# Performance work log

Measured on AMD Instinct MI355X. Metric: run time of the kernel, lower is better.

## Reference

```python
import jax, jax.numpy as jnp
import numpy as np

N = 50000      # nodes per graph
E = 800000     # edges per graph (avg degree 16)
IN = 128       # in_channels == hidden_channels
HID = 128      # out_channels (heads=1)
R = 8          # num_relations
NEG = 0.2      # PyG RGATConv default negative_slope


def setup_inputs() -> dict:
    key = jax.random.key(0)
    ks = jax.random.split(key, 14)
    s_w = (2.0 / (IN + HID)) ** 0.5  # glorot-ish scale
    return {
        "x_one": jax.random.normal(ks[0], (N, IN), jnp.float32),
        "edge_index_one": jax.random.randint(ks[1], (2, E), 0, N),
        "edge_type_one": jax.random.randint(ks[2], (E,), 0, R),
        "x_two": jax.random.normal(ks[3], (N, IN), jnp.float32),
        "edge_index_two": jax.random.randint(ks[4], (2, E), 0, N),
        "edge_type_two": jax.random.randint(ks[5], (E,), 0, R),
        "W1": jax.random.normal(ks[6], (R, IN, HID), jnp.float32) * s_w,
        "q1": jax.random.normal(ks[7], (HID, 1), jnp.float32) * s_w,
        "k1": jax.random.normal(ks[8], (HID, 1), jnp.float32) * s_w,
        "b1": jnp.zeros((HID,), jnp.float32),
        "W2": jax.random.normal(ks[9], (R, IN, HID), jnp.float32) * s_w,
        "q2": jax.random.normal(ks[10], (HID, 1), jnp.float32) * s_w,
        "k2": jax.random.normal(ks[11], (HID, 1), jnp.float32) * s_w,
        "b2": jnp.zeros((HID,), jnp.float32),
    }


def _rgat(x, edge_index, edge_type, W, q, k, b):
    """PyG RGATConv (heads=1, additive-self-attention, across-relation)."""
    n = x.shape[0]
    src, dst = edge_index[0], edge_index[1]
    # per-relation linear transform of all nodes: [R, N, HID]
    xt = jnp.einsum('nd,rdo->rno', x, W)
    out_i = xt[edge_type, dst]   # [E, HID] transformed target (x_i W_r)
    out_j = xt[edge_type, src]   # [E, HID] transformed source (x_j W_r)
    qi = out_i @ q               # [E, 1]
    kj = out_j @ k               # [E, 1]
    alpha = jax.nn.leaky_relu(qi + kj, NEG)
    # scatter-softmax over incoming edges of each dst node
    amax = jax.ops.segment_max(alpha, dst, num_segments=n)
    amax = jnp.where(jnp.isfinite(amax), amax, 0.0)
    ex = jnp.exp(alpha - amax[dst])
    denom = jax.ops.segment_sum(ex, dst, num_segments=n) + 1e-16
    a = ex / denom[dst]          # [E, 1]
    # weighted scatter-add aggregation + bias
    out = jax.ops.segment_sum(a * out_j, dst, num_segments=n) + b
    return out


def reference(x_one, edge_index_one, edge_type_one,
              x_two, edge_index_two, edge_type_two,
              W1, q1, k1, b1, W2, q2, k2, b2):
    o1 = jax.nn.relu(_rgat(x_one, edge_index_one, edge_type_one, W1, q1, k1, b1))
    o2 = jax.nn.relu(_rgat(x_two, edge_index_two, edge_type_two, W2, q2, k2, b2))
    return (o1, o2)
```

## Files before the change

kernel.cpp:

```cpp
#include <hip/hip_runtime.h>


typedef unsigned short u16;
typedef __attribute__((ext_vector_type(8))) short short8;
typedef __attribute__((ext_vector_type(4))) float floatx4;
typedef __attribute__((ext_vector_type(4))) float float4v;
typedef __attribute__((ext_vector_type(4))) unsigned uint4v;

__device__ __forceinline__ u16 f2bf(float f) {
  union { float f; unsigned u; } v; v.f = f;
  unsigned r = v.u + 0x7FFFu + ((v.u >> 16) & 1u);
  return (u16)(r >> 16);
}
__device__ __forceinline__ float bflo(unsigned v) {
  union { unsigned u; float f; } c; c.u = v << 16; return c.f;
}
__device__ __forceinline__ float bfhi(unsigned v) {
  union { unsigned u; float f; } c; c.u = v & 0xffff0000u; return c.f;
}

__global__ void k_prep_wb(const float* __restrict__ W1, const float* __restrict__ W2,
                          u16* __restrict__ Wb, int KK) {
  int t = blockIdx.x * 256 + threadIdx.x;
  int lane = t & 63, nt = (t >> 6) & 7, kk = t >> 9;
  if (kk >= KK) return;
  const float* W = blockIdx.y ? W2 : W1;
  u16* out = Wb + (size_t)blockIdx.y * KK * 4096;
  int q = lane >> 4, m16 = lane & 15;
  int c = nt * 16 + m16;
  short8 v;
#pragma unroll
  for (int j = 0; j < 8; ++j) {
    int k = kk * 32 + q * 8 + j;
    v[j] = (short)f2bf(W[(size_t)k * 128 + c]);
  }
  *(short8*)(out + (size_t)t * 8) = v;
}

__global__ void k_prep_wqk(const float* __restrict__ W1, const float* __restrict__ q1,
                           const float* __restrict__ k1, const float* __restrict__ W2,
                           const float* __restrict__ q2, const float* __restrict__ k2,
                           float* __restrict__ Wq, float* __restrict__ Wk, int RD) {
  int wid = (blockIdx.x * 256 + threadIdx.x) >> 6;
  int lane = threadIdx.x & 63;
  if (wid >= 2 * RD) return;
  int g = wid >= RD;
  const float* W = g ? W2 : W1;
  const float* qv = g ? q2 : q1;
  const float* kv = g ? k2 : k1;
  const float* row = W + (size_t)(wid - g * RD) * 128;
  float a0 = row[lane], a1 = row[lane + 64];
  float vq = a0 * qv[lane] + a1 * qv[lane + 64];
  float vk = a0 * kv[lane] + a1 * kv[lane + 64];
#pragma unroll
  for (int off = 32; off; off >>= 1) {
    vq += __shfl_xor(vq, off);
    vk += __shfl_xor(vk, off);
  }
  if (lane == 0) { Wq[wid] = vq; Wk[wid] = vk; }
}

__global__ void k_prep_bqk(const float* __restrict__ Wq, const float* __restrict__ Wk,
                           u16* __restrict__ Bqk, int R) {
  int total = 2 * 4 * 64 * 8;
  for (int idx = threadIdx.x; idx < total; idx += 256) {
    int j = idx & 7, lane = (idx >> 3) & 63, kk = (idx >> 9) & 3, g = idx >> 11;
    int k = kk * 32 + ((lane >> 4) & 3) * 8 + j;
    int n = lane & 15;
    float v = (n < 8) ? Wq[(g * R + n) * 128 + k] : Wk[(g * R + (n & 7)) * 128 + k];
    Bqk[idx] = f2bf(v);
  }
}

__global__ void __launch_bounds__(256) k_count(
    const int* __restrict__ d1, const int* __restrict__ d2,
    int* __restrict__ gcnt, int N, int E, int NB) {
  __shared__ int h[512];
  int tid = threadIdx.x;
  for (int i = tid; i < NB; i += 256) h[i] = 0;
  __syncthreads();
  int E2 = 2 * E;
  int e0 = blockIdx.x * 4096;
#pragma unroll
  for (int j = 0; j < 16; ++j) {
    int e = e0 + j * 256 + tid;
    if (e < E2) {
      int g = e >= E;
      int d = g ? d2[e - E] : d1[e];
      atomicAdd(&h[(g * N + d) >> 8], 1);
    }
  }
  __syncthreads();
  for (int i = tid; i < NB; i += 256)
    if (h[i]) atomicAdd(&gcnt[i], h[i]);
}

__global__ void k_bucket_scan(const int* __restrict__ gcnt, int* __restrict__ bbase,
                              int* __restrict__ bcur, int* __restrict__ offs,
                              int NB, int total, int N2) {
  __shared__ int sd[512];
  int tid = threadIdx.x;
  int v0 = (tid < NB) ? gcnt[tid] : 0;
  int v1 = (tid + 256 < NB) ? gcnt[tid + 256] : 0;
  sd[tid] = v0; sd[tid + 256] = v1;
  __syncthreads();
  for (int off = 1; off < 512; off <<= 1) {
    int t0 = (tid >= off) ? sd[tid - off] : 0;
    int t1 = (tid + 256 >= off) ? sd[tid + 256 - off] : 0;
    __syncthreads();
    sd[tid] += t0; sd[tid + 256] += t1;
    __syncthreads();
  }
  if (tid < NB) { int b = sd[tid] - v0; bbase[tid] = b; bcur[tid] = b; }
  if (tid + 256 < NB) { int b = sd[tid + 256] - v1; bbase[tid + 256] = b; bcur[tid + 256] = b; }
  if (tid == 0) { bbase[NB] = total; offs[N2] = total; }
}

__global__ void __launch_bounds__(256) k_bin(
    const int* __restrict__ ei1, const int* __restrict__ et1,
    const int* __restrict__ ei2, const int* __restrict__ et2,
    int* __restrict__ bcur, uint2* __restrict__ staged, int N, int E, int NB) {
  __shared__ int hist[512];
  __shared__ int basev[512];
  __shared__ int runstart[512];
  __shared__ unsigned sta[4096 * 2];
  int tid = threadIdx.x;
  int E2 = 2 * E;
  int e0 = blockIdx.x * 4096;
  int cnt2 = min(4096, E2 - e0);
  for (int i = tid; i < 512; i += 256) hist[i] = 0;
  __syncthreads();
  int dstg[16], srcet[16], rank[16];
#pragma unroll
  for (int j = 0; j < 16; ++j) {
    int e = e0 + j * 256 + tid;
    dstg[j] = -1;
    if (e < E2) {
      int g = e >= E;
      int el = e - (g ? E : 0);
      const int* ei = g ? ei2 : ei1;
      int s = ei[el], d = ei[E + el];
      int etv = (g ? et2 : et1)[el];
      dstg[j] = g * N + d;
      srcet[j] = (s << 3) | etv;
      rank[j] = atomicAdd(&hist[dstg[j] >> 8], 1);
    }
  }
  __syncthreads();
  basev[tid] = hist[tid];
  basev[tid + 256] = hist[tid + 256];
  __syncthreads();
  for (int off = 1; off < 512; off <<= 1) {
    int i0 = tid, i1 = tid + 256;
    int v0 = (i0 >= off) ? basev[i0 - off] : 0;
    int v1 = (i1 >= off) ? basev[i1 - off] : 0;
    __syncthreads();
    basev[i0] += v0; basev[i1] += v1;
    __syncthreads();
  }
  for (int i = tid; i < NB; i += 256)
    if (hist[i] > 0) runstart[i] = atomicAdd(&bcur[i], hist[i]);
  __syncthreads();
#pragma unroll
  for (int j = 0; j < 16; ++j)
    if (dstg[j] >= 0) {
      int b = dstg[j] >> 8;
      int slot = basev[b] - hist[b] + rank[j];
      sta[slot * 2] = (unsigned)dstg[j];
      sta[slot * 2 + 1] = (unsigned)srcet[j];
    }
  __syncthreads();
  for (int i = tid; i < cnt2; i += 256) {
    unsigned dg = sta[i * 2], se = sta[i * 2 + 1];
    int b = (int)(dg >> 8);
    int dest = runstart[b] + (i - (basev[b] - hist[b]));
    staged[dest] = make_uint2(dg, se);
  }
}

__global__ void __launch_bounds__(256) k_scatter2(
    const uint2* __restrict__ staged, const int* __restrict__ bbase,
    int* __restrict__ offs, int* __restrict__ csr, int N2) {
  __shared__ int hist[256];
  __shared__ int sd[256];
  __shared__ int cur[256];
  int b = blockIdx.x, tid = threadIdx.x;
  int nb0 = b << 8;
  int nnode = min(256, N2 - nb0);
  int s0 = bbase[b], s1 = bbase[b + 1];
  hist[tid] = 0;
  __syncthreads();
  for (int i = s0 + tid; i < s1; i += 256)
    atomicAdd(&hist[(int)staged[i].x - nb0], 1);
  __syncthreads();
  int v = hist[tid];
  sd[tid] = v; __syncthreads();
  for (int off = 1; off < 256; off <<= 1) {
    int t = (tid >= off) ? sd[tid - off] : 0;
    __syncthreads();
    sd[tid] += t;
    __syncthreads();
  }
  int ex = sd[tid] - v;
  if (tid < nnode) offs[nb0 + tid] = s0 + ex;
  cur[tid] = ex;
  __syncthreads();
  for (int i = s0 + tid; i < s1; i += 256) {
    uint2 en = staged[i];
    int node = (int)en.x - nb0;
    int sl = atomicAdd(&cur[node], 1);
    csr[s0 + sl] = (int)en.y;
  }
}

__global__ void __launch_bounds__(256) k_gemm_xt(
    const float* __restrict__ x, const u16* __restrict__ Wb,
    const u16* __restrict__ Bqk, u16* __restrict__ xt,
    float* __restrict__ sq, float* __restrict__ sk,
    int N, int R, int node_base) {
  __shared__ u16 st[4][2][2048];
  int wave = threadIdx.x >> 6, lane = threadIdx.x & 63;
  int m0 = blockIdx.x * 64 + wave * 16;
  int rbase = blockIdx.y * 4;
  int q = lane >> 4, m16 = lane & 15;
  int node = m0 + m16;
  int srow = (node < N) ? node : N - 1;
  short8 bfrag[4];
#pragma unroll
  for (int kk = 0; kk < 4; ++kk) {
    const float* ap = x + (size_t)srow * 128 + kk * 32 + q * 8;
    float4v f0 = *(const float4v*)ap;
    float4v f1 = *(const float4v*)(ap + 4);
    short8 a;
    a[0] = (short)f2bf(f0.x); a[1] = (short)f2bf(f0.y);
    a[2] = (short)f2bf(f0.z); a[3] = (short)f2bf(f0.w);
    a[4] = (short)f2bf(f1.x); a[5] = (short)f2bf(f1.y);
    a[6] = (short)f2bf(f1.z); a[7] = (short)f2bf(f1.w);
    bfrag[kk] = a;
  }
  if (blockIdx.y == 0) {
    floatx4 accq = (floatx4){0.f, 0.f, 0.f, 0.f};
#pragma unroll
    for (int kk = 0; kk < 4; ++kk) {
      short8 aq = *(const short8*)(Bqk + (size_t)kk * 512 + lane * 8);
      accq = __builtin_amdgcn_mfma_f32_16x16x32_bf16(aq, bfrag[kk], accq, 0, 0, 0);
    }
    if (node < N) {
      float* dst = (q < 2 ? sq : sk) + (size_t)(node_base + node) * 8 + (q & 1) * 4;
      *(float4v*)dst = (float4v){accq[0], accq[1], accq[2], accq[3]};
    }
  }
#pragma unroll
  for (int rr = 0; rr < 4; ++rr) {
    int r = rbase + rr;
    u16* s = st[wave][rr & 1];
    floatx4 acc[8];
#pragma unroll
    for (int nt = 0; nt < 8; ++nt) acc[nt] = (floatx4){0.f, 0.f, 0.f, 0.f};
#pragma unroll
    for (int kk = 0; kk < 4; ++kk) {
      const u16* wbp = Wb + ((size_t)((r * 4 + kk) * 8) * 64 + lane) * 8;
#pragma unroll
      for (int nt = 0; nt < 8; ++nt) {
        short8 a = *(const short8*)(wbp + nt * 512);
        acc[nt] = __builtin_amdgcn_mfma_f32_16x16x32_bf16(a, bfrag[kk], acc[nt], 0, 0, 0);
      }
    }
#pragma unroll
    for (int nt = 0; nt < 8; ++nt) {
      union { u16 h[4]; unsigned long long u; } pk;
      pk.h[0] = f2bf(acc[nt][0]); pk.h[1] = f2bf(acc[nt][1]);
      pk.h[2] = f2bf(acc[nt][2]); pk.h[3] = f2bf(acc[nt][3]);
      int c16 = 2 * nt + (q >> 1);
      *(unsigned long long*)(s + (((m16 << 4) + (c16 ^ m16)) << 3) + ((q & 1) << 2)) = pk.u;
    }
#pragma unroll
    for (int it = 0; it < 4; ++it) {
      int rl = it * 4 + q;
      int gm = m0 + rl;
      if (gm < N) {
        uint4v vv = *(const uint4v*)(s + (((rl << 4) + (m16 ^ rl)) << 3));
        *(uint4v*)(xt + ((size_t)r * N + gm) * 128 + m16 * 8) = vv;
      }
    }
  }
}

__global__ void __launch_bounds__(256) k_aggregate(
    const int* __restrict__ csr, const int* __restrict__ offs,
    const float* __restrict__ sq, const float* __restrict__ sk,
    const u16* __restrict__ xt, const float* __restrict__ bias,
    float* __restrict__ out, int N, int node_base) {
  int nl = blockIdx.x * 4 + (threadIdx.x >> 6);
  int lane = threadIdx.x & 63;
  if (nl >= N) return;
  int node = node_base + nl;
  int start = offs[node], end = offs[node + 1];
  const float* sqn = sq + (size_t)node * 8;

  float al[8]; int pl[8];
  float m = -INFINITY;
  {
    int c = 0;
    for (int i = start + lane; i < end; i += 64, ++c) {
      int p = csr[i]; int s = p >> 3, e = p & 7;
      float a = sqn[e] + sk[(size_t)(node_base + s) * 8 + e];
      a = (a > 0.f) ? a : 0.2f * a;
      if (c < 8) { al[c] = a; pl[c] = p; }
      m = fmaxf(m, a);
    }
  }
#pragma unroll
  for (int off = 32; off; off >>= 1) m = fmaxf(m, __shfl_xor(m, off));

  float ssum = 0.f;
  {
    int c = 0;
    for (int i = start + lane; i < end; i += 64, ++c) {
      float a;
      if (c < 8) a = al[c];
      else {
        int p = csr[i]; int s = p >> 3, e = p & 7;
        a = sqn[e] + sk[(size_t)(node_base + s) * 8 + e];
        a = (a > 0.f) ? a : 0.2f * a;
      }
      ssum += __expf(a - m);
    }
  }
#pragma unroll
  for (int off = 32; off; off >>= 1) ssum += __shfl_xor(ssum, off);
  float inv = 1.f / (ssum + 1e-16f);

  float acc0 = 0.f, acc1 = 0.f;
  const char* xtb = (const char*)xt;
  int c = 0;
  for (int base = start; base < end; base += 64, ++c) {
    int cnt = min(64, end - base);
    float w = 0.f; int b = 0;
    {
      int i = base + lane;
      if (i < end) {
        int p; float a;
        if (c < 8) { p = pl[c]; a = al[c]; }
        else {
          p = csr[i]; int s = p >> 3, e = p & 7;
          a = sqn[e] + sk[(size_t)(node_base + s) * 8 + e];
          a = (a > 0.f) ? a : 0.2f * a;
        }
        w = __expf(a - m) * inv;
        b = ((p & 7) * N + (p >> 3)) << 8;
      }
    }
    int j = 0;
    for (; j + 3 < cnt; j += 4) {
      float w0 = __shfl(w, j), w1 = __shfl(w, j + 1),
            w2 = __shfl(w, j + 2), w3 = __shfl(w, j + 3);
      int b0 = __shfl(b, j), b1 = __shfl(b, j + 1),
          b2 = __shfl(b, j + 2), b3 = __shfl(b, j + 3);
      unsigned v0 = *(const unsigned*)(xtb + b0 + lane * 4);
      unsigned v1 = *(const unsigned*)(xtb + b1 + lane * 4);
      unsigned v2 = *(const unsigned*)(xtb + b2 + lane * 4);
      unsigned v3 = *(const unsigned*)(xtb + b3 + lane * 4);
      acc0 += w0 * bflo(v0); acc1 += w0 * bfhi(v0);
      acc0 += w1 * bflo(v1); acc1 += w1 * bfhi(v1);
      acc0 += w2 * bflo(v2); acc1 += w2 * bfhi(v2);
      acc0 += w3 * bflo(v3); acc1 += w3 * bfhi(v3);
    }
    for (; j < cnt; ++j) {
      float w0 = __shfl(w, j);
      int b0 = __shfl(b, j);
      unsigned v0 = *(const unsigned*)(xtb + b0 + lane * 4);
      acc0 += w0 * bflo(v0); acc1 += w0 * bfhi(v0);
    }
  }
  float o0 = fmaxf(acc0 + bias[lane * 2], 0.f);
  float o1 = fmaxf(acc1 + bias[lane * 2 + 1], 0.f);
  union { float f[2]; unsigned long long u; } pk;
  pk.f[0] = o0; pk.f[1] = o1;
  __builtin_nontemporal_store(pk.u,
      (unsigned long long*)(out + (size_t)nl * 128 + lane * 2));
}

extern "C" void kernel_launch(void* const* d_in, const int* in_sizes, int n_in,
                              void* d_out, int out_size, void* d_ws, size_t ws_size,
                              hipStream_t stream) {
  const float* x1 = (const float*)d_in[0];
  const int* ei1 = (const int*)d_in[1];
  const int* et1 = (const int*)d_in[2];
  const float* x2 = (const float*)d_in[3];
  const int* ei2 = (const int*)d_in[4];
  const int* et2 = (const int*)d_in[5];
  const float* W1 = (const float*)d_in[6];
  const float* q1 = (const float*)d_in[7];
  const float* k1 = (const float*)d_in[8];
  const float* b1 = (const float*)d_in[9];
  const float* W2 = (const float*)d_in[10];
  const float* q2 = (const float*)d_in[11];
  const float* k2 = (const float*)d_in[12];
  const float* b2 = (const float*)d_in[13];

  const int N = in_sizes[0] / 128;
  const int E = in_sizes[1] / 2;
  const int R = in_sizes[6] / (128 * 128);
  const int KK = R * 4;
  const int N2 = 2 * N;
  const int NB = (N2 + 255) >> 8;

  size_t off = 0;
  char* w = (char*)d_ws;
  auto carve = [&](size_t bytes) -> void* {
    void* p = w + off;
    off += (bytes + 255) & ~(size_t)255;
    return p;
  };
  u16* xt = (u16*)carve((size_t)R * N * 128 * 2);
  uint2* staged = (uint2*)xt;
  u16* Wb = (u16*)carve((size_t)2 * KK * 4096 * 2);
  u16* Bqk = (u16*)carve((size_t)2 * 4 * 64 * 8 * 2);
  float* Wq = (float*)carve((size_t)2 * R * 128 * 4);
  float* Wk = (float*)carve((size_t)2 * R * 128 * 4);
  float* sq = (float*)carve((size_t)N2 * 8 * 4);
  float* sk = (float*)carve((size_t)N2 * 8 * 4);
  int* offs = (int*)carve((size_t)(N2 + 1) * 4);
  int* gcnt = (int*)carve(512 * 4);
  int* bbase = (int*)carve(520 * 4);
  int* bcur = (int*)carve(512 * 4);
  int* csr = (int*)carve((size_t)2 * E * 4);
  if (off > ws_size) return;

  const int nbin = (2 * E + 4095) / 4096;

  hipMemsetAsync(gcnt, 0, 512 * 4, stream);
  k_prep_wb<<<dim3((KK * 512 + 255) / 256, 2), dim3(256), 0, stream>>>(W1, W2, Wb, KK);
  k_prep_wqk<<<dim3((2 * R * 128 * 64 + 255) / 256), dim3(256), 0, stream>>>(
      W1, q1, k1, W2, q2, k2, Wq, Wk, R * 128);
  k_prep_bqk<<<dim3(1), dim3(256), 0, stream>>>(Wq, Wk, Bqk, R);
  k_count<<<dim3(nbin), dim3(256), 0, stream>>>(ei1 + E, ei2 + E, gcnt, N, E, NB);
  k_bucket_scan<<<dim3(1), dim3(256), 0, stream>>>(gcnt, bbase, bcur, offs, NB, 2 * E, N2);
  k_bin<<<dim3(nbin), dim3(256), 0, stream>>>(ei1, et1, ei2, et2, bcur, staged, N, E, NB);
  k_scatter2<<<dim3(NB), dim3(256), 0, stream>>>(staged, bbase, offs, csr, N2);

  for (int g = 0; g < 2; ++g) {
    const float* x = g ? x2 : x1;
    const float* bv = g ? b2 : b1;
    float* outp = (float*)d_out + (size_t)g * N * 128;
    k_gemm_xt<<<dim3((N + 63) / 64, 2), dim3(256), 0, stream>>>(
        x, Wb + (size_t)g * KK * 4096, Bqk + (size_t)g * 2048, xt,
        sq, sk, N, R, g * N);
    k_aggregate<<<dim3((N + 3) / 4), dim3(256), 0, stream>>>(
        csr, offs, sq, sk, xt, bv, outp, N, g * N);
  }
}
```

Measured before the change: 356.1 us.

## Replace bucketed two-pass CSR build with per-node count, scan and atomic placement

The CSR build used a two-level scheme: coarse bucket histograms, LDS-staged binning into 256-node buckets, then a per-bucket scatter pass. It becomes per-node global atomic counts, a three-kernel exclusive scan over 100k nodes, and a single placement pass using global atomics on per-node cursors. This removes the staged intermediate buffer and its extra read/write pass. In exchange it adds more global atomics and kernel launches, and edge order within each node becomes nondeterministic, which may change float summation order and aggregation locality.

```diff
diff --git a/kernel.cpp b/kernel.cpp
--- a/kernel.cpp
+++ b/kernel.cpp
@@ -74,34 +74,45 @@
 
 __global__ void __launch_bounds__(256) k_count(
     const int* __restrict__ d1, const int* __restrict__ d2,
-    int* __restrict__ gcnt, int N, int E, int NB) {
-  __shared__ int h[512];
-  int tid = threadIdx.x;
-  for (int i = tid; i < NB; i += 256) h[i] = 0;
-  __syncthreads();
+    int* __restrict__ nodecnt, int N, int E) {
   int E2 = 2 * E;
   int e0 = blockIdx.x * 4096;
 #pragma unroll
   for (int j = 0; j < 16; ++j) {
-    int e = e0 + j * 256 + tid;
+    int e = e0 + j * 256 + threadIdx.x;
     if (e < E2) {
       int g = e >= E;
       int d = g ? d2[e - E] : d1[e];
-      atomicAdd(&h[(g * N + d) >> 8], 1);
-    }
-  }
+      atomicAdd(&nodecnt[g * N + d], 1);
+    }
+  }
+}
+
+__global__ void __launch_bounds__(256) k_scan1(
+    const int* __restrict__ nodecnt, int* __restrict__ exls,
+    int* __restrict__ bsum, int N2) {
+  __shared__ int sd[256];
+  int tid = threadIdx.x;
+  int n = (blockIdx.x << 8) + tid;
+  int v = (n < N2) ? nodecnt[n] : 0;
+  sd[tid] = v;
   __syncthreads();
-  for (int i = tid; i < NB; i += 256)
-    if (h[i]) atomicAdd(&gcnt[i], h[i]);
-}
-
-__global__ void k_bucket_scan(const int* __restrict__ gcnt, int* __restrict__ bbase,
-                              int* __restrict__ bcur, int* __restrict__ offs,
-                              int NB, int total, int N2) {
+  for (int off = 1; off < 256; off <<= 1) {
+    int t = (tid >= off) ? sd[tid - off] : 0;
+    __syncthreads();
+    sd[tid] += t;
+    __syncthreads();
+  }
+  if (n < N2) exls[n] = sd[tid] - v;
+  if (tid == 255) bsum[blockIdx.x] = sd[255];
+}
+
+__global__ void k_scan2(const int* __restrict__ bsum, int* __restrict__ bbase,
+                        int* __restrict__ offs, int NB, int total, int N2) {
   __shared__ int sd[512];
   int tid = threadIdx.x;
-  int v0 = (tid < NB) ? gcnt[tid] : 0;
-  int v1 = (tid + 256 < NB) ? gcnt[tid + 256] : 0;
+  int v0 = (tid < NB) ? bsum[tid] : 0;
+  int v1 = (tid + 256 < NB) ? bsum[tid + 256] : 0;
   sd[tid] = v0; sd[tid + 256] = v1;
   __syncthreads();
   for (int off = 1; off < 512; off <<= 1) {
@@ -111,105 +122,40 @@
     sd[tid] += t0; sd[tid + 256] += t1;
     __syncthreads();
   }
-  if (tid < NB) { int b = sd[tid] - v0; bbase[tid] = b; bcur[tid] = b; }
-  if (tid + 256 < NB) { int b = sd[tid + 256] - v1; bbase[tid + 256] = b; bcur[tid + 256] = b; }
+  if (tid < NB) bbase[tid] = sd[tid] - v0;
+  if (tid + 256 < NB) bbase[tid + 256] = sd[tid + 256] - v1;
   if (tid == 0) { bbase[NB] = total; offs[N2] = total; }
 }
 
-__global__ void __launch_bounds__(256) k_bin(
+__global__ void __launch_bounds__(256) k_scan3(
+    const int* __restrict__ exls, const int* __restrict__ bbase,
+    int* __restrict__ offs, int* __restrict__ cur, int N2) {
+  int n = (blockIdx.x << 8) + threadIdx.x;
+  if (n < N2) {
+    int v = bbase[blockIdx.x] + exls[n];
+    offs[n] = v;
+    cur[n] = v;
+  }
+}
+
+__global__ void __launch_bounds__(256) k_place(
     const int* __restrict__ ei1, const int* __restrict__ et1,
     const int* __restrict__ ei2, const int* __restrict__ et2,
-    int* __restrict__ bcur, uint2* __restrict__ staged, int N, int E, int NB) {
-  __shared__ int hist[512];
-  __shared__ int basev[512];
-  __shared__ int runstart[512];
-  __shared__ unsigned sta[4096 * 2];
-  int tid = threadIdx.x;
+    int* __restrict__ cur, int* __restrict__ csr, int N, int E) {
   int E2 = 2 * E;
   int e0 = blockIdx.x * 4096;
-  int cnt2 = min(4096, E2 - e0);
-  for (int i = tid; i < 512; i += 256) hist[i] = 0;
-  __syncthreads();
-  int dstg[16], srcet[16], rank[16];
 #pragma unroll
   for (int j = 0; j < 16; ++j) {
-    int e = e0 + j * 256 + tid;
-    dstg[j] = -1;
+    int e = e0 + j * 256 + threadIdx.x;
     if (e < E2) {
       int g = e >= E;
       int el = e - (g ? E : 0);
       const int* ei = g ? ei2 : ei1;
       int s = ei[el], d = ei[E + el];
       int etv = (g ? et2 : et1)[el];
-      dstg[j] = g * N + d;
-      srcet[j] = (s << 3) | etv;
-      rank[j] = atomicAdd(&hist[dstg[j] >> 8], 1);
-    }
-  }
-  __syncthreads();
-  basev[tid] = hist[tid];
-  basev[tid + 256] = hist[tid + 256];
-  __syncthreads();
-  for (int off = 1; off < 512; off <<= 1) {
-    int i0 = tid, i1 = tid + 256;
-    int v0 = (i0 >= off) ? basev[i0 - off] : 0;
-    int v1 = (i1 >= off) ? basev[i1 - off] : 0;
-    __syncthreads();
-    basev[i0] += v0; basev[i1] += v1;
-    __syncthreads();
-  }
-  for (int i = tid; i < NB; i += 256)
-    if (hist[i] > 0) runstart[i] = atomicAdd(&bcur[i], hist[i]);
-  __syncthreads();
-#pragma unroll
-  for (int j = 0; j < 16; ++j)
-    if (dstg[j] >= 0) {
-      int b = dstg[j] >> 8;
-      int slot = basev[b] - hist[b] + rank[j];
-      sta[slot * 2] = (unsigned)dstg[j];
-      sta[slot * 2 + 1] = (unsigned)srcet[j];
-    }
-  __syncthreads();
-  for (int i = tid; i < cnt2; i += 256) {
-    unsigned dg = sta[i * 2], se = sta[i * 2 + 1];
-    int b = (int)(dg >> 8);
-    int dest = runstart[b] + (i - (basev[b] - hist[b]));
-    staged[dest] = make_uint2(dg, se);
-  }
-}
-
-__global__ void __launch_bounds__(256) k_scatter2(
-    const uint2* __restrict__ staged, const int* __restrict__ bbase,
-    int* __restrict__ offs, int* __restrict__ csr, int N2) {
-  __shared__ int hist[256];
-  __shared__ int sd[256];
-  __shared__ int cur[256];
-  int b = blockIdx.x, tid = threadIdx.x;
-  int nb0 = b << 8;
-  int nnode = min(256, N2 - nb0);
-  int s0 = bbase[b], s1 = bbase[b + 1];
-  hist[tid] = 0;
-  __syncthreads();
-  for (int i = s0 + tid; i < s1; i += 256)
-    atomicAdd(&hist[(int)staged[i].x - nb0], 1);
-  __syncthreads();
-  int v = hist[tid];
-  sd[tid] = v; __syncthreads();
-  for (int off = 1; off < 256; off <<= 1) {
-    int t = (tid >= off) ? sd[tid - off] : 0;
-    __syncthreads();
-    sd[tid] += t;
-    __syncthreads();
-  }
-  int ex = sd[tid] - v;
-  if (tid < nnode) offs[nb0 + tid] = s0 + ex;
-  cur[tid] = ex;
-  __syncthreads();
-  for (int i = s0 + tid; i < s1; i += 256) {
-    uint2 en = staged[i];
-    int node = (int)en.x - nb0;
-    int sl = atomicAdd(&cur[node], 1);
-    csr[s0 + sl] = (int)en.y;
+      int slot = atomicAdd(&cur[g * N + d], 1);
+      csr[slot] = (s << 3) | etv;
+    }
   }
 }
 
@@ -414,7 +360,6 @@
     return p;
   };
   u16* xt = (u16*)carve((size_t)R * N * 128 * 2);
-  uint2* staged = (uint2*)xt;
   u16* Wb = (u16*)carve((size_t)2 * KK * 4096 * 2);
   u16* Bqk = (u16*)carve((size_t)2 * 4 * 64 * 8 * 2);
   float* Wq = (float*)carve((size_t)2 * R * 128 * 4);
@@ -422,23 +367,26 @@
   float* sq = (float*)carve((size_t)N2 * 8 * 4);
   float* sk = (float*)carve((size_t)N2 * 8 * 4);
   int* offs = (int*)carve((size_t)(N2 + 1) * 4);
-  int* gcnt = (int*)carve(512 * 4);
+  int* nodecnt = (int*)carve((size_t)N2 * 4);
+  int* exls = (int*)carve((size_t)N2 * 4);
+  int* cur = (int*)carve((size_t)N2 * 4);
+  int* bsum = (int*)carve(512 * 4);
   int* bbase = (int*)carve(520 * 4);
-  int* bcur = (int*)carve(512 * 4);
   int* csr = (int*)carve((size_t)2 * E * 4);
   if (off > ws_size) return;
 
   const int nbin = (2 * E + 4095) / 4096;
 
-  hipMemsetAsync(gcnt, 0, 512 * 4, stream);
+  hipMemsetAsync(nodecnt, 0, (size_t)N2 * 4, stream);
   k_prep_wb<<<dim3((KK * 512 + 255) / 256, 2), dim3(256), 0, stream>>>(W1, W2, Wb, KK);
   k_prep_wqk<<<dim3((2 * R * 128 * 64 + 255) / 256), dim3(256), 0, stream>>>(
       W1, q1, k1, W2, q2, k2, Wq, Wk, R * 128);
   k_prep_bqk<<<dim3(1), dim3(256), 0, stream>>>(Wq, Wk, Bqk, R);
-  k_count<<<dim3(nbin), dim3(256), 0, stream>>>(ei1 + E, ei2 + E, gcnt, N, E, NB);
-  k_bucket_scan<<<dim3(1), dim3(256), 0, stream>>>(gcnt, bbase, bcur, offs, NB, 2 * E, N2);
-  k_bin<<<dim3(nbin), dim3(256), 0, stream>>>(ei1, et1, ei2, et2, bcur, staged, N, E, NB);
-  k_scatter2<<<dim3(NB), dim3(256), 0, stream>>>(staged, bbase, offs, csr, N2);
+  k_count<<<dim3(nbin), dim3(256), 0, stream>>>(ei1 + E, ei2 + E, nodecnt, N, E);
+  k_scan1<<<dim3(NB), dim3(256), 0, stream>>>(nodecnt, exls, bsum, N2);
+  k_scan2<<<dim3(1), dim3(256), 0, stream>>>(bsum, bbase, offs, NB, 2 * E, N2);
+  k_scan3<<<dim3(NB), dim3(256), 0, stream>>>(exls, bbase, offs, cur, N2);
+  k_place<<<dim3(nbin), dim3(256), 0, stream>>>(ei1, et1, ei2, et2, cur, csr, N, E);
 
   for (int g = 0; g < 2; ++g) {
     const float* x = g ? x2 : x1;
```

After: 489.6 us. +37.5%, slower.

## Batch both graphs into single GEMM and aggregate launches, fuse Wq/Wk prep

Applied to the files above, without the earlier changes.

When the workspace can hold two copies of the transformed node features, the two graphs are processed by one k_gemm_xt launch and one k_aggregate launch, with the graph index taken from a grid dimension. Otherwise the old per-graph loop is kept. The Wq/Wk projection and Bqk packing kernels are merged into a single multi-block kernel, and f32-to-bf16 conversion now uses the packed v_cvt_pk_bf16_f32 instruction. This cuts launch count and serialization between graphs and gives each launch more parallelism, at the cost of twice the workspace for xt and less L2 reuse per graph.

```diff
diff --git a/kernel.cpp b/kernel.cpp
--- a/kernel.cpp
+++ b/kernel.cpp
@@ -17,6 +17,11 @@
 }
 __device__ __forceinline__ float bfhi(unsigned v) {
   union { unsigned u; float f; } c; c.u = v & 0xffff0000u; return c.f;
+}
+__device__ __forceinline__ unsigned cvtpk(float lo, float hi) {
+  unsigned r;
+  asm("v_cvt_pk_bf16_f32 %0, %1, %2" : "=v"(r) : "v"(lo), "v"(hi));
+  return r;
 }
 
 __global__ void k_prep_wb(const float* __restrict__ W1, const float* __restrict__ W2,
@@ -37,39 +42,26 @@
   *(short8*)(out + (size_t)t * 8) = v;
 }
 
-__global__ void k_prep_wqk(const float* __restrict__ W1, const float* __restrict__ q1,
-                           const float* __restrict__ k1, const float* __restrict__ W2,
-                           const float* __restrict__ q2, const float* __restrict__ k2,
-                           float* __restrict__ Wq, float* __restrict__ Wk, int RD) {
-  int wid = (blockIdx.x * 256 + threadIdx.x) >> 6;
-  int lane = threadIdx.x & 63;
-  if (wid >= 2 * RD) return;
-  int g = wid >= RD;
+__global__ void __launch_bounds__(256) k_prep_bqk(
+    const float* __restrict__ W1, const float* __restrict__ q1,
+    const float* __restrict__ k1, const float* __restrict__ W2,
+    const float* __restrict__ q2, const float* __restrict__ k2,
+    u16* __restrict__ Bqk) {
+  int idx = blockIdx.x * 256 + threadIdx.x;
+  int j = idx & 7, lane = (idx >> 3) & 63, kk = (idx >> 9) & 3, g = idx >> 11;
+  int k = kk * 32 + ((lane >> 4) & 3) * 8 + j;
+  int n = lane & 15;
   const float* W = g ? W2 : W1;
-  const float* qv = g ? q2 : q1;
-  const float* kv = g ? k2 : k1;
-  const float* row = W + (size_t)(wid - g * RD) * 128;
-  float a0 = row[lane], a1 = row[lane + 64];
-  float vq = a0 * qv[lane] + a1 * qv[lane + 64];
-  float vk = a0 * kv[lane] + a1 * kv[lane + 64];
-#pragma unroll
-  for (int off = 32; off; off >>= 1) {
-    vq += __shfl_xor(vq, off);
-    vk += __shfl_xor(vk, off);
-  }
-  if (lane == 0) { Wq[wid] = vq; Wk[wid] = vk; }
-}
-
-__global__ void k_prep_bqk(const float* __restrict__ Wq, const float* __restrict__ Wk,
-                           u16* __restrict__ Bqk, int R) {
-  int total = 2 * 4 * 64 * 8;
-  for (int idx = threadIdx.x; idx < total; idx += 256) {
-    int j = idx & 7, lane = (idx >> 3) & 63, kk = (idx >> 9) & 3, g = idx >> 11;
-    int k = kk * 32 + ((lane >> 4) & 3) * 8 + j;
-    int n = lane & 15;
-    float v = (n < 8) ? Wq[(g * R + n) * 128 + k] : Wk[(g * R + (n & 7)) * 128 + k];
-    Bqk[idx] = f2bf(v);
-  }
+  const float* vec = (n < 8) ? (g ? q2 : q1) : (g ? k2 : k1);
+  const float* row = W + ((size_t)(n & 7) * 128 + k) * 128;
+  float s = 0.f;
+#pragma unroll
+  for (int o = 0; o < 128; o += 4) {
+    float4v wv = *(const float4v*)(row + o);
+    float4v qv = *(const float4v*)(vec + o);
+    s += wv.x * qv.x + wv.y * qv.y + wv.z * qv.z + wv.w * qv.w;
+  }
+  Bqk[idx] = f2bf(s);
 }
 
 __global__ void __launch_bounds__(256) k_count(
@@ -214,11 +206,18 @@
 }
 
 __global__ void __launch_bounds__(256) k_gemm_xt(
-    const float* __restrict__ x, const u16* __restrict__ Wb,
-    const u16* __restrict__ Bqk, u16* __restrict__ xt,
+    const float* __restrict__ x1, const float* __restrict__ x2,
+    const u16* __restrict__ Wb, const u16* __restrict__ Bqk,
+    u16* __restrict__ xt, unsigned long long xt_gstride,
     float* __restrict__ sq, float* __restrict__ sk,
-    int N, int R, int node_base) {
+    int N, int R, int g0) {
   __shared__ u16 st[4][2][2048];
+  int g = g0 + blockIdx.z;
+  const float* x = g ? x2 : x1;
+  const u16* Wbg = Wb + (size_t)g * (R * 4) * 4096;
+  const u16* Bqkg = Bqk + (size_t)g * 2048;
+  u16* xtg = xt + (size_t)g * xt_gstride;
+  int node_base = g * N;
   int wave = threadIdx.x >> 6, lane = threadIdx.x & 63;
   int m0 = blockIdx.x * 64 + wave * 16;
   int rbase = blockIdx.y * 4;
@@ -231,18 +230,16 @@
     const float* ap = x + (size_t)srow * 128 + kk * 32 + q * 8;
     float4v f0 = *(const float4v*)ap;
     float4v f1 = *(const float4v*)(ap + 4);
-    short8 a;
-    a[0] = (short)f2bf(f0.x); a[1] = (short)f2bf(f0.y);
-    a[2] = (short)f2bf(f0.z); a[3] = (short)f2bf(f0.w);
-    a[4] = (short)f2bf(f1.x); a[5] = (short)f2bf(f1.y);
-    a[6] = (short)f2bf(f1.z); a[7] = (short)f2bf(f1.w);
-    bfrag[kk] = a;
+    union { unsigned u[4]; short8 s; } pb;
+    pb.u[0] = cvtpk(f0.x, f0.y); pb.u[1] = cvtpk(f0.z, f0.w);
+    pb.u[2] = cvtpk(f1.x, f1.y); pb.u[3] = cvtpk(f1.z, f1.w);
+    bfrag[kk] = pb.s;
   }
   if (blockIdx.y == 0) {
     floatx4 accq = (floatx4){0.f, 0.f, 0.f, 0.f};
 #pragma unroll
     for (int kk = 0; kk < 4; ++kk) {
-      short8 aq = *(const short8*)(Bqk + (size_t)kk * 512 + lane * 8);
+      short8 aq = *(const short8*)(Bqkg + (size_t)kk * 512 + lane * 8);
       accq = __builtin_amdgcn_mfma_f32_16x16x32_bf16(aq, bfrag[kk], accq, 0, 0, 0);
     }
     if (node < N) {
@@ -259,7 +256,7 @@
     for (int nt = 0; nt < 8; ++nt) acc[nt] = (floatx4){0.f, 0.f, 0.f, 0.f};
 #pragma unroll
     for (int kk = 0; kk < 4; ++kk) {
-      const u16* wbp = Wb + ((size_t)((r * 4 + kk) * 8) * 64 + lane) * 8;
+      const u16* wbp = Wbg + ((size_t)((r * 4 + kk) * 8) * 64 + lane) * 8;
 #pragma unroll
       for (int nt = 0; nt < 8; ++nt) {
         short8 a = *(const short8*)(wbp + nt * 512);
@@ -268,11 +265,11 @@
     }
 #pragma unroll
     for (int nt = 0; nt < 8; ++nt) {
-      union { u16 h[4]; unsigned long long u; } pk;
-      pk.h[0] = f2bf(acc[nt][0]); pk.h[1] = f2bf(acc[nt][1]);
-      pk.h[2] = f2bf(acc[nt][2]); pk.h[3] = f2bf(acc[nt][3]);
+      union { unsigned u[2]; unsigned long long ull; } pk;
+      pk.u[0] = cvtpk(acc[nt][0], acc[nt][1]);
+      pk.u[1] = cvtpk(acc[nt][2], acc[nt][3]);
       int c16 = 2 * nt + (q >> 1);
-      *(unsigned long long*)(s + (((m16 << 4) + (c16 ^ m16)) << 3) + ((q & 1) << 2)) = pk.u;
+      *(unsigned long long*)(s + (((m16 << 4) + (c16 ^ m16)) << 3) + ((q & 1) << 2)) = pk.ull;
     }
 #pragma unroll
     for (int it = 0; it < 4; ++it) {
@@ -280,7 +277,7 @@
       int gm = m0 + rl;
       if (gm < N) {
         uint4v vv = *(const uint4v*)(s + (((rl << 4) + (m16 ^ rl)) << 3));
-        *(uint4v*)(xt + ((size_t)r * N + gm) * 128 + m16 * 8) = vv;
+        *(uint4v*)(xtg + ((size_t)r * N + gm) * 128 + m16 * 8) = vv;
       }
     }
   }
@@ -289,11 +286,17 @@
 __global__ void __launch_bounds__(256) k_aggregate(
     const int* __restrict__ csr, const int* __restrict__ offs,
     const float* __restrict__ sq, const float* __restrict__ sk,
-    const u16* __restrict__ xt, const float* __restrict__ bias,
-    float* __restrict__ out, int N, int node_base) {
+    const u16* __restrict__ xt, unsigned long long xt_gstride,
+    const float* __restrict__ b1, const float* __restrict__ b2,
+    float* __restrict__ out, int N, int g0) {
   int nl = blockIdx.x * 4 + (threadIdx.x >> 6);
   int lane = threadIdx.x & 63;
   if (nl >= N) return;
+  int g = g0 + blockIdx.y;
+  int node_base = g * N;
+  const float* bias = g ? b2 : b1;
+  const u16* xtg = xt + (size_t)g * xt_gstride;
+  float* outp = out + (size_t)g * N * 128;
   int node = node_base + nl;
   int start = offs[node], end = offs[node + 1];
   const float* sqn = sq + (size_t)node * 8;
@@ -332,7 +335,7 @@
   float inv = 1.f / (ssum + 1e-16f);
 
   float acc0 = 0.f, acc1 = 0.f;
-  const char* xtb = (const char*)xt;
+  const char* xtb = (const char*)xtg;
   int c = 0;
   for (int base = start; base < end; base += 64, ++c) {
     int cnt = min(64, end - base);
@@ -355,11 +358,11 @@
     for (; j + 3 < cnt; j += 4) {
       float w0 = __shfl(w, j), w1 = __shfl(w, j + 1),
             w2 = __shfl(w, j + 2), w3 = __shfl(w, j + 3);
-      int b0 = __shfl(b, j), b1 = __shfl(b, j + 1),
-          b2 = __shfl(b, j + 2), b3 = __shfl(b, j + 3);
+      int b0 = __shfl(b, j), b1_ = __shfl(b, j + 1),
+          b2_ = __shfl(b, j + 2), b3 = __shfl(b, j + 3);
       unsigned v0 = *(const unsigned*)(xtb + b0 + lane * 4);
-      unsigned v1 = *(const unsigned*)(xtb + b1 + lane * 4);
-      unsigned v2 = *(const unsigned*)(xtb + b2 + lane * 4);
+      unsigned v1 = *(const unsigned*)(xtb + b1_ + lane * 4);
+      unsigned v2 = *(const unsigned*)(xtb + b2_ + lane * 4);
       unsigned v3 = *(const unsigned*)(xtb + b3 + lane * 4);
       acc0 += w0 * bflo(v0); acc1 += w0 * bfhi(v0);
       acc0 += w1 * bflo(v1); acc1 += w1 * bfhi(v1);
@@ -378,7 +381,7 @@
   union { float f[2]; unsigned long long u; } pk;
   pk.f[0] = o0; pk.f[1] = o1;
   __builtin_nontemporal_store(pk.u,
-      (unsigned long long*)(out + (size_t)nl * 128 + lane * 2));
+      (unsigned long long*)(outp + (size_t)nl * 128 + lane * 2));
 }
 
 extern "C" void kernel_launch(void* const* d_in, const int* in_sizes, int n_in,
@@ -413,12 +416,8 @@
     off += (bytes + 255) & ~(size_t)255;
     return p;
   };
-  u16* xt = (u16*)carve((size_t)R * N * 128 * 2);
-  uint2* staged = (uint2*)xt;
   u16* Wb = (u16*)carve((size_t)2 * KK * 4096 * 2);
   u16* Bqk = (u16*)carve((size_t)2 * 4 * 64 * 8 * 2);
-  float* Wq = (float*)carve((size_t)2 * R * 128 * 4);
-  float* Wk = (float*)carve((size_t)2 * R * 128 * 4);
   float* sq = (float*)carve((size_t)N2 * 8 * 4);
   float* sk = (float*)carve((size_t)N2 * 8 * 4);
   int* offs = (int*)carve((size_t)(N2 + 1) * 4);
@@ -426,28 +425,34 @@
   int* bbase = (int*)carve(520 * 4);
   int* bcur = (int*)carve(512 * 4);
   int* csr = (int*)carve((size_t)2 * E * 4);
-  if (off > ws_size) return;
+  size_t xt_elems = (size_t)R * N * 128;
+  u16* xt = (u16*)(w + off);
+  bool merged = (off + 2 * xt_elems * 2) <= ws_size;
+  if (off + xt_elems * 2 > ws_size) return;
+  uint2* staged = (uint2*)xt;
+  unsigned long long gstride = merged ? (unsigned long long)xt_elems : 0ull;
 
   const int nbin = (2 * E + 4095) / 4096;
 
   hipMemsetAsync(gcnt, 0, 512 * 4, stream);
   k_prep_wb<<<dim3((KK * 512 + 255) / 256, 2), dim3(256), 0, stream>>>(W1, W2, Wb, KK);
-  k_prep_wqk<<<dim3((2 * R * 128 * 64 + 255) / 256), dim3(256), 0, stream>>>(
-      W1, q1, k1, W2, q2, k2, Wq, Wk, R * 128);
-  k_prep_bqk<<<dim3(1), dim3(256), 0, stream>>>(Wq, Wk, Bqk, R);
+  k_prep_bqk<<<dim3(16), dim3(256), 0, stream>>>(W1, q1, k1, W2, q2, k2, Bqk);
   k_count<<<dim3(nbin), dim3(256), 0, stream>>>(ei1 + E, ei2 + E, gcnt, N, E, NB);
   k_bucket_scan<<<dim3(1), dim3(256), 0, stream>>>(gcnt, bbase, bcur, offs, NB, 2 * E, N2);
   k_bin<<<dim3(nbin), dim3(256), 0, stream>>>(ei1, et1, ei2, et2, bcur, staged, N, E, NB);
   k_scatter2<<<dim3(NB), dim3(256), 0, stream>>>(staged, bbase, offs, csr, N2);
 
-  for (int g = 0; g < 2; ++g) {
-    const float* x = g ? x2 : x1;
-    const float* bv = g ? b2 : b1;
-    float* outp = (float*)d_out + (size_t)g * N * 128;
-    k_gemm_xt<<<dim3((N + 63) / 64, 2), dim3(256), 0, stream>>>(
-        x, Wb + (size_t)g * KK * 4096, Bqk + (size_t)g * 2048, xt,
-        sq, sk, N, R, g * N);
-    k_aggregate<<<dim3((N + 3) / 4), dim3(256), 0, stream>>>(
-        csr, offs, sq, sk, xt, bv, outp, N, g * N);
-  }
-}
+  if (merged) {
+    k_gemm_xt<<<dim3((N + 63) / 64, 2, 2), dim3(256), 0, stream>>>(
+        x1, x2, Wb, Bqk, xt, gstride, sq, sk, N, R, 0);
+    k_aggregate<<<dim3((N + 3) / 4, 2), dim3(256), 0, stream>>>(
+        csr, offs, sq, sk, xt, gstride, b1, b2, (float*)d_out, N, 0);
+  } else {
+    for (int g = 0; g < 2; ++g) {
+      k_gemm_xt<<<dim3((N + 63) / 64, 2, 1), dim3(256), 0, stream>>>(
+          x1, x2, Wb, Bqk, xt, 0ull, sq, sk, N, R, g);
+      k_aggregate<<<dim3((N + 3) / 4, 1), dim3(256), 0, stream>>>(
+          csr, offs, sq, sk, xt, 0ull, b1, b2, (float*)d_out, N, g);
+    }
+  }
+}
```

Result: no change. 362.5 us (+1.8%).
